# Kernel optimization log

Hardware: AMD Instinct MI355X
Metric: run time of the kernel (lower is better)

Reference implementation:

```python
import jax, jax.numpy as jnp
import numpy as np

DIM, NHEADS, HEAD_DIM = 1536, 12, 128
EPS = 1e-6
ROPE_SPLIT = (22, 21, 21)  # head_dim//2 = 64 -> (c-2*(c//3), c//3, c//3)


def setup_inputs() -> dict:
    key = jax.random.key(0)
    ks = jax.random.split(key, 12)
    B, F, H, W = 1, 8, 16, 28
    L = F * H * W  # 3584
    inp = {
        "x": jax.random.normal(ks[0], (B, L, DIM), jnp.float32),
        "seq_lens": jnp.full((B,), L, dtype=jnp.int64),
        "grid_sizes": jnp.array([[F, H, W]] * B, dtype=jnp.int64),
        "freqs": jax.random.uniform(ks[1], (1024, HEAD_DIM // 2), jnp.float32) * (2 * np.pi),
        "Wq": jax.random.normal(ks[2], (DIM, DIM), jnp.float32) / np.sqrt(DIM),
        "bq": jnp.zeros((DIM,), jnp.float32),
        "Wk": jax.random.normal(ks[3], (DIM, DIM), jnp.float32) / np.sqrt(DIM),
        "bk": jnp.zeros((DIM,), jnp.float32),
        "Wv": jax.random.normal(ks[4], (DIM, DIM), jnp.float32) / np.sqrt(DIM),
        "bv": jnp.zeros((DIM,), jnp.float32),
        "Wo": jax.random.normal(ks[5], (DIM, DIM), jnp.float32) / np.sqrt(DIM),
        "bo": jnp.zeros((DIM,), jnp.float32),
        "gq": jnp.ones((DIM,), jnp.float32),
        "gk": jnp.ones((DIM,), jnp.float32),
    }
    return inp


def _rms_norm(x, g):
    var = jnp.mean(jnp.square(x), axis=-1, keepdims=True)
    return x * jax.lax.rsqrt(var + EPS) * g


def _rope_angles(freqs, F, H, W):
    # freqs: [1024, 64] angles; split per 3D axis and broadcast over the grid
    cf, ch, cw = ROPE_SPLIT
    af = freqs[:F, :cf]
    ah = freqs[:H, cf:cf + ch]
    aw = freqs[:W, cf + ch:]
    ang = jnp.concatenate([
        jnp.broadcast_to(af[:, None, None, :], (F, H, W, cf)),
        jnp.broadcast_to(ah[None, :, None, :], (F, H, W, ch)),
        jnp.broadcast_to(aw[None, None, :, :], (F, H, W, cw)),
    ], axis=-1).reshape(F * H * W, cf + ch + cw)  # [L, 64]
    return jnp.cos(ang), jnp.sin(ang)


def _rope_apply(x, cos, sin):
    # x: [B, L, N, D]; complex multiply by unit-modulus freqs, in real arithmetic
    b, s, n, d = x.shape
    xr = x.reshape(b, s, n, d // 2, 2)
    a, bi = xr[..., 0], xr[..., 1]
    c = cos[None, :, None, :]
    si = sin[None, :, None, :]
    out = jnp.stack([a * c - bi * si, a * si + bi * c], axis=-1)
    return out.reshape(b, s, n, d)


def reference(x, seq_lens, grid_sizes, freqs, Wq, bq, Wk, bk, Wv, bv, Wo, bo, gq, gk):
    b, s, _ = x.shape
    n, d = NHEADS, HEAD_DIM
    gs = np.asarray(grid_sizes)
    F, H, W = int(gs[0, 0]), int(gs[0, 1]), int(gs[0, 2])  # static grid (same per batch)

    q = _rms_norm(x @ Wq + bq, gq).reshape(b, s, n, d)
    k = _rms_norm(x @ Wk + bk, gk).reshape(b, s, n, d)
    v = (x @ Wv + bv).reshape(b, s, n, d)

    cos, sin = _rope_angles(freqs, F, H, W)
    q = _rope_apply(q, cos, sin)
    k = _rope_apply(k, cos, sin)

    # full attention with key-length masking (flash_attention k_lens semantics)
    scale = 1.0 / np.sqrt(d)
    scores = jnp.einsum("bqnd,bknd->bnqk", q, k) * scale
    key_mask = jnp.arange(s)[None, :] < seq_lens[:, None]  # [B, S]
    scores = jnp.where(key_mask[:, None, None, :], scores, -1e9)
    probs = jax.nn.softmax(scores, axis=-1)
    out = jnp.einsum("bnqk,bknd->bqnd", probs, v)

    return out.reshape(b, s, n * d) @ Wo + bo
```

## Files before the change

kernel.cpp:

```cpp
#include <hip/hip_runtime.h>

typedef __bf16 bf16;
typedef __bf16 bf16x8 __attribute__((ext_vector_type(8)));
typedef __bf16 bf16x4 __attribute__((ext_vector_type(4)));
typedef float f32x4 __attribute__((ext_vector_type(4)));

__device__ __forceinline__ void gload_lds16(const void* g, void* l) {
  __builtin_amdgcn_global_load_lds(
      (const __attribute__((address_space(1))) void*)g,
      (__attribute__((address_space(3))) void*)l, 16, 0, 0);
}

__device__ __forceinline__ bf16x8 ld8(const bf16* p) {
  bf16x8 v; __builtin_memcpy(&v, p, 16); return v;
}

__global__ __launch_bounds__(256) void cast_f32_bf16(const float* __restrict__ in,
                                                     bf16* __restrict__ out, int n8) {
  int i = blockIdx.x * 256 + threadIdx.x;
  if (i >= n8) return;
  const float4* p = (const float4*)in + (size_t)i * 2;
  float4 a = p[0], b = p[1];
  bf16x8 o;
  o[0] = (bf16)a.x; o[1] = (bf16)a.y; o[2] = (bf16)a.z; o[3] = (bf16)a.w;
  o[4] = (bf16)b.x; o[5] = (bf16)b.y; o[6] = (bf16)b.z; o[7] = (bf16)b.w;
  *((bf16x8*)out + i) = o;
}

__global__ __launch_bounds__(256) void transpose_w(const float* __restrict__ W,
                                                   bf16* __restrict__ Wt) {
  __shared__ bf16 tile[64][72];
  int t = threadIdx.x;
  int k0 = blockIdx.x * 64, n0 = blockIdx.y * 64;
  int r = t >> 2, c0 = (t & 3) * 16;
  const float* src = W + (size_t)(k0 + r) * 1536 + n0 + c0;
#pragma unroll
  for (int q = 0; q < 4; ++q) {
    float4 v = *(const float4*)(src + q * 4);
    tile[c0 + q * 4 + 0][r] = (bf16)v.x;
    tile[c0 + q * 4 + 1][r] = (bf16)v.y;
    tile[c0 + q * 4 + 2][r] = (bf16)v.z;
    tile[c0 + q * 4 + 3][r] = (bf16)v.w;
  }
  __syncthreads();
  bf16* dst = Wt + (size_t)(n0 + r) * 1536 + k0 + c0;
  bf16x8 o0, o1;
#pragma unroll
  for (int j = 0; j < 8; ++j) { o0[j] = tile[r][c0 + j]; o1[j] = tile[r][c0 + 8 + j]; }
  *(bf16x8*)dst = o0;
  *(bf16x8*)(dst + 8) = o1;
}

__global__ void concat_bias(const float* __restrict__ bq, const float* __restrict__ bk,
                            const float* __restrict__ bv, float* __restrict__ o) {
  int t = blockIdx.x * 256 + threadIdx.x;
  if (t < 1536) o[t] = bq[t];
  else if (t < 3072) o[t] = bk[t - 1536];
  else if (t < 4608) o[t] = bv[t - 3072];
}

template <typename OUT>
__global__ __launch_bounds__(256, 2) void gemm_bt(const bf16* __restrict__ A, const bf16* __restrict__ B,
                                                  const float* __restrict__ bias, OUT* __restrict__ C,
                                                  int M, int N, int K) {
  __shared__ bf16 As[128 * 32], Bs[128 * 32];
  int t = threadIdx.x, l = t & 63, w = t >> 6;
  int lane15 = l & 15, lhi = l >> 4;
  int m0 = blockIdx.x * 128, n0 = blockIdx.y * 128;
  int wm = (w >> 1) * 64, wn = (w & 1) * 64;
  f32x4 zero = {0.f, 0.f, 0.f, 0.f};
  f32x4 acc[4][4];
#pragma unroll
  for (int i = 0; i < 4; ++i)
#pragma unroll
    for (int j = 0; j < 4; ++j) acc[i][j] = zero;

  int srow = t >> 2, scol = (t & 3) * 8;
  const bf16* gA0 = A + (size_t)(m0 + srow) * K + scol;
  const bf16* gA1 = A + (size_t)(m0 + 64 + srow) * K + scol;
  const bf16* gB0 = B + (size_t)(n0 + srow) * K + scol;
  const bf16* gB1 = B + (size_t)(n0 + 64 + srow) * K + scol;
  char* ldsA = (char*)As + (size_t)w * 1024;
  char* ldsB = (char*)Bs + (size_t)w * 1024;

  for (int kt = 0; kt < K; kt += 32) {
    gload_lds16(gA0 + kt, ldsA);
    gload_lds16(gA1 + kt, ldsA + 4096);
    gload_lds16(gB0 + kt, ldsB);
    gload_lds16(gB1 + kt, ldsB + 4096);
    __syncthreads();
    bf16x8 af[4], bfr[4];
#pragma unroll
    for (int i = 0; i < 4; ++i) {
      af[i]  = ld8(&As[(wm + i * 16 + lane15) * 32 + lhi * 8]);
      bfr[i] = ld8(&Bs[(wn + i * 16 + lane15) * 32 + lhi * 8]);
    }
#pragma unroll
    for (int i = 0; i < 4; ++i)
#pragma unroll
      for (int j = 0; j < 4; ++j)
        acc[i][j] = __builtin_amdgcn_mfma_f32_16x16x32_bf16(af[i], bfr[j], acc[i][j], 0, 0, 0);
    __syncthreads();
  }
#pragma unroll
  for (int i = 0; i < 4; ++i)
#pragma unroll
    for (int j = 0; j < 4; ++j) {
      int col = n0 + wn + j * 16 + lane15;
      float bb = bias[col];
#pragma unroll
      for (int r = 0; r < 4; ++r) {
        int row = m0 + wm + i * 16 + lhi * 4 + r;
        C[(size_t)row * N + col] = (OUT)(acc[i][j][r] + bb);
      }
    }
}

__global__ void rope_tab(const float* __restrict__ freqs, const int* __restrict__ gs,
                         float* __restrict__ tabc, float* __restrict__ tabs) {
  int idx = blockIdx.x * 256 + threadIdx.x;
  if (idx >= 3584 * 64) return;
  int s = idx >> 6, i = idx & 63;
  int H = gs[1], W = gs[2];
  int f = s / (H * W);
  int rem = s - f * (H * W);
  int hh = rem / W;
  int ww = rem - hh * W;
  int row = (i < 22) ? f : ((i < 43) ? hh : ww);
  float a = freqs[row * 64 + i];
  tabc[idx] = cosf(a);
  tabs[idx] = sinf(a);
}

__global__ __launch_bounds__(256) void postproc(const bf16* __restrict__ QKV,
    const float* __restrict__ gq, const float* __restrict__ gk,
    const float* __restrict__ tabc, const float* __restrict__ tabs,
    bf16* __restrict__ qb, bf16* __restrict__ kb) {
  int s = blockIdx.x, t = threadIdx.x;
  const bf16* Qr = QKV + (size_t)s * 4608;
  const bf16* Kr = Qr + 1536;
  int j0 = t * 6;
  float qv[6], kv[6];
  float sq = 0.f, sk = 0.f;
#pragma unroll
  for (int j = 0; j < 6; ++j) {
    float a = (float)Qr[j0 + j]; qv[j] = a; sq += a * a;
    float b = (float)Kr[j0 + j]; kv[j] = b; sk += b * b;
  }
#pragma unroll
  for (int off = 32; off > 0; off >>= 1) {
    sq += __shfl_down(sq, off);
    sk += __shfl_down(sk, off);
  }
  __shared__ float red[2][4];
  if ((t & 63) == 0) { red[0][t >> 6] = sq; red[1][t >> 6] = sk; }
  __syncthreads();
  float vq = (red[0][0] + red[0][1]) + (red[0][2] + red[0][3]);
  float vk = (red[1][0] + red[1][1]) + (red[1][2] + red[1][3]);
  float rq = 1.0f / sqrtf(vq * (1.0f / 1536.0f) + 1e-6f);
  float rk = 1.0f / sqrtf(vk * (1.0f / 1536.0f) + 1e-6f);
#pragma unroll
  for (int j = 0; j < 6; j += 2) {
    int jj = j0 + j;
    int d = jj & 127, i = d >> 1, h = jj >> 7;
    float c = tabc[s * 64 + i], sn = tabs[s * 64 + i];
    size_t base = (((size_t)h * 3584 + s) << 7) + d;
    float a = qv[j] * rq * gq[jj], b = qv[j + 1] * rq * gq[jj + 1];
    qb[base] = (bf16)(a * c - b * sn);
    qb[base + 1] = (bf16)(a * sn + b * c);
    float ak = kv[j] * rk * gk[jj], bk2 = kv[j + 1] * rk * gk[jj + 1];
    kb[base] = (bf16)(ak * c - bk2 * sn);
    kb[base + 1] = (bf16)(ak * sn + bk2 * c);
  }
}

__global__ __launch_bounds__(256) void transpose_v(const bf16* __restrict__ QKV,
                                                   bf16* __restrict__ vT) {
  __shared__ bf16 tile[128][72];
  int t = threadIdx.x;
  int h = blockIdx.y;
  int s0 = blockIdx.x * 64;
  int r = t >> 2, c0 = (t & 3) * 32;
  const bf16* src = QKV + (size_t)(s0 + r) * 4608 + 3072 + h * 128 + c0;
#pragma unroll
  for (int q = 0; q < 4; ++q) {
    bf16x8 v = ld8(src + q * 8);
#pragma unroll
    for (int j = 0; j < 8; ++j) tile[c0 + q * 8 + j][r] = v[j];
  }
  __syncthreads();
  int d = t >> 1, sp = (t & 1) * 32;
  bf16* dst = vT + (size_t)(h * 128 + d) * 3584 + s0 + sp;
#pragma unroll
  for (int q = 0; q < 4; ++q) {
    bf16x8 o;
#pragma unroll
    for (int j = 0; j < 8; ++j) o[j] = tile[d][sp + q * 8 + j];
    *(bf16x8*)(dst + q * 8) = o;
  }
}

__global__ __launch_bounds__(256, 2) void flash_attn(
    const bf16* __restrict__ qb, const bf16* __restrict__ kb, const bf16* __restrict__ vT,
    const int* __restrict__ sl, float* __restrict__ po0, float* __restrict__ po1,
    float* __restrict__ po2, float* __restrict__ po3, float* __restrict__ ml) {
  const int L = 3584;
  __shared__ bf16 Ks[2][64 * 128];
  __shared__ bf16 Vs[2][128 * 64];
  int t = threadIdx.x, l = t & 63, w = t >> 6;
  int lane15 = l & 15, lhi = l >> 4;
  int grp48 = l & 48;
  int h = blockIdx.y, z = blockIdx.z;
  int qw = blockIdx.x * 128 + w * 32;
  int seqlen = sl[0];
  const float scale = 0.08838834764831845f;
  float* po = (z == 0) ? po0 : (z == 1) ? po1 : (z == 2) ? po2 : po3;
  float* mlz = ml + (size_t)z * 12 * L * 2;

  bf16x8 aq[2][4];
#pragma unroll
  for (int qf = 0; qf < 2; ++qf)
#pragma unroll
    for (int kc = 0; kc < 4; ++kc)
      aq[qf][kc] = ld8(qb + (((size_t)h * L + qw + qf * 16 + lane15) << 7) + kc * 32 + lhi * 8);

  f32x4 zero = {0.f, 0.f, 0.f, 0.f};
  f32x4 out[2][8];
  float m2[2] = {-1e30f, -1e30f}, ls2[2] = {0.f, 0.f};
#pragma unroll
  for (int qf = 0; qf < 2; ++qf)
#pragma unroll
    for (int df = 0; df < 8; ++df) out[qf][df] = zero;

  int nt = (seqlen + 63) >> 6;
  if (nt > 56) nt = 56;
  int t0 = z * 14, t1 = t0 + 14;
  if (t0 > nt) t0 = nt;
  if (t1 > nt) t1 = nt;

  int rk_s = t >> 4, ck_s = (t & 15) * 16;
  int rv_s = t >> 3;
  int mm = t & 7;
  int sA = 32 * (mm >> 2) + 16 * (mm & 1) + 4 * ((mm >> 1) & 1);
  int oA = 2 * sA;
  int swzk = (rk_s & 7) << 4;
  int swzv = (rv_s & 7) << 4;

  bf16x8 kreg[4], vreg[4];
  if (t0 < t1) {
    int kv0 = t0 * 64;
#pragma unroll
    for (int p = 0; p < 4; ++p) {
      kreg[p] = ld8(kb + (((size_t)h * L + kv0 + p * 16 + rk_s) << 7) + (ck_s >> 1));
      vreg[p] = ld8(vT + (size_t)(h * 128 + p * 32 + rv_s) * L + kv0 + mm * 8);
    }
  }

  int buf = 0;
  for (int ti = t0; ti < t1; ++ti) {
    int kv0 = ti * 64;
#pragma unroll
    for (int p = 0; p < 4; ++p) {
      __builtin_memcpy((char*)Ks[buf] + (p * 16 + rk_s) * 256 + (ck_s ^ swzk), &kreg[p], 16);
      bf16x4 lo, hi;
#pragma unroll
      for (int j = 0; j < 4; ++j) { lo[j] = vreg[p][j]; hi[j] = vreg[p][j + 4]; }
      char* vrow = (char*)Vs[buf] + (p * 32 + rv_s) * 128;
      __builtin_memcpy(vrow + (oA ^ swzv), &lo, 8);
      __builtin_memcpy(vrow + ((oA + 16) ^ swzv), &hi, 8);
    }
    if (ti + 1 < t1) {
      int kn = (ti + 1) * 64;
#pragma unroll
      for (int p = 0; p < 4; ++p) {
        kreg[p] = ld8(kb + (((size_t)h * L + kn + p * 16 + rk_s) << 7) + (ck_s >> 1));
        vreg[p] = ld8(vT + (size_t)(h * 128 + p * 32 + rv_s) * L + kn + mm * 8);
      }
    }
    __syncthreads();

    f32x4 sc[2][4];
#pragma unroll
    for (int qf = 0; qf < 2; ++qf)
#pragma unroll
      for (int a = 0; a < 4; ++a) sc[qf][a] = zero;
#pragma unroll
    for (int a = 0; a < 4; ++a) {
      int rk = a * 16 + lane15;
      const char* krow = (const char*)Ks[buf] + rk * 256;
      int swz = (rk & 7) << 4;
#pragma unroll
      for (int kc = 0; kc < 4; ++kc) {
        bf16x8 bk_ = ld8((const bf16*)(krow + ((kc * 64 + lhi * 16) ^ swz)));
        sc[0][a] = __builtin_amdgcn_mfma_f32_16x16x32_bf16(bk_, aq[0][kc], sc[0][a], 0, 0, 0);
        sc[1][a] = __builtin_amdgcn_mfma_f32_16x16x32_bf16(bk_, aq[1][kc], sc[1][a], 0, 0, 0);
      }
    }

    bool full = (kv0 + 64 <= seqlen);
    bf16x8 ap[2][2];
#pragma unroll
    for (int qf = 0; qf < 2; ++qf) {
      float tm = -1e30f;
#pragma unroll
      for (int a = 0; a < 4; ++a)
#pragma unroll
        for (int r = 0; r < 4; ++r) {
          float s = sc[qf][a][r] * scale;
          if (!full) {
            int col = kv0 + a * 16 + lhi * 4 + r;
            s = (col < seqlen) ? s : -1e30f;
          }
          sc[qf][a][r] = s;
          tm = fmaxf(tm, s);
        }
      tm = fmaxf(tm, __shfl_xor(tm, 16));
      tm = fmaxf(tm, __shfl_xor(tm, 32));
      if (!__all(tm <= m2[qf] + 8.0f)) {
        float nm = fmaxf(m2[qf], tm);
        float f = __expf(m2[qf] - nm);
        m2[qf] = nm;
        ls2[qf] *= f;
#pragma unroll
        for (int r = 0; r < 4; ++r) {
          float fr = __shfl(f, grp48 | (lhi * 4 + r));
#pragma unroll
          for (int df = 0; df < 8; ++df) out[qf][df][r] *= fr;
        }
      }
      float psum = 0.f;
#pragma unroll
      for (int a = 0; a < 4; ++a)
#pragma unroll
        for (int r = 0; r < 4; ++r) {
          float p = __expf(sc[qf][a][r] - m2[qf]);
          sc[qf][a][r] = p;
          psum += p;
        }
      psum += __shfl_xor(psum, 16);
      psum += __shfl_xor(psum, 32);
      ls2[qf] += psum;
#pragma unroll
      for (int c = 0; c < 2; ++c) {
        bf16x8 f8;
#pragma unroll
        for (int r = 0; r < 4; ++r) {
          f8[r] = (bf16)sc[qf][2 * c][r];
          f8[r + 4] = (bf16)sc[qf][2 * c + 1][r];
        }
        ap[qf][c] = f8;
      }
    }

#pragma unroll
    for (int df = 0; df < 8; ++df) {
      int rd = df * 16 + lane15;
      const char* vrow2 = (const char*)Vs[buf] + rd * 128;
      int swz = (rd & 7) << 4;
#pragma unroll
      for (int c = 0; c < 2; ++c) {
        bf16x8 bv_ = ld8((const bf16*)(vrow2 + ((c * 64 + lhi * 16) ^ swz)));
        out[0][df] = __builtin_amdgcn_mfma_f32_16x16x32_bf16(ap[0][c], bv_, out[0][df], 0, 0, 0);
        out[1][df] = __builtin_amdgcn_mfma_f32_16x16x32_bf16(ap[1][c], bv_, out[1][df], 0, 0, 0);
      }
    }
    buf ^= 1;
  }

#pragma unroll
  for (int qf = 0; qf < 2; ++qf) {
#pragma unroll
    for (int r = 0; r < 4; ++r) {
      int row = qw + qf * 16 + lhi * 4 + r;
      size_t rbase = ((size_t)h * L + row) << 7;
#pragma unroll
      for (int df = 0; df < 8; ++df)
        po[rbase + df * 16 + lane15] = out[qf][df][r];
    }
    if (lhi == 0) {
      int row = qw + qf * 16 + lane15;
      mlz[(((size_t)h * L + row) << 1)] = m2[qf];
      mlz[(((size_t)h * L + row) << 1) + 1] = ls2[qf];
    }
  }
}

__global__ __launch_bounds__(256) void combine4(
    const float* __restrict__ po0, const float* __restrict__ po1,
    const float* __restrict__ po2, const float* __restrict__ po3,
    const float* __restrict__ ml, bf16* __restrict__ attn) {
  const int L = 3584;
  int row = blockIdx.x * 8 + (threadIdx.x >> 5);
  int c0 = (threadIdx.x & 31) * 4;
  const size_t mls = (size_t)12 * L * 2;
  float m0 = ml[row * 2],           l0 = ml[row * 2 + 1];
  float m1 = ml[mls + row * 2],     l1 = ml[mls + row * 2 + 1];
  float m2 = ml[2 * mls + row * 2], l2 = ml[2 * mls + row * 2 + 1];
  float m3 = ml[3 * mls + row * 2], l3 = ml[3 * mls + row * 2 + 1];
  float M = fmaxf(fmaxf(m0, m1), fmaxf(m2, m3));
  float w0 = __expf(m0 - M), w1 = __expf(m1 - M);
  float w2 = __expf(m2 - M), w3 = __expf(m3 - M);
  float inv = 1.0f / fmaxf(w0 * l0 + w1 * l1 + w2 * l2 + w3 * l3, 1e-30f);
  float4 a = *(const float4*)(po0 + (size_t)row * 128 + c0);
  float4 b = *(const float4*)(po1 + (size_t)row * 128 + c0);
  float4 c = *(const float4*)(po2 + (size_t)row * 128 + c0);
  float4 d = *(const float4*)(po3 + (size_t)row * 128 + c0);
  int h = row / L, s = row % L;
  bf16x4 o;
  o[0] = (bf16)((w0 * a.x + w1 * b.x + w2 * c.x + w3 * d.x) * inv);
  o[1] = (bf16)((w0 * a.y + w1 * b.y + w2 * c.y + w3 * d.y) * inv);
  o[2] = (bf16)((w0 * a.z + w1 * b.z + w2 * c.z + w3 * d.z) * inv);
  o[3] = (bf16)((w0 * a.w + w1 * b.w + w2 * c.w + w3 * d.w) * inv);
  *(bf16x4*)(attn + (size_t)s * 1536 + h * 128 + c0) = o;
}

extern "C" void kernel_launch(void* const* d_in, const int* in_sizes, int n_in,
                              void* d_out, int out_size, void* d_ws, size_t ws_size,
                              hipStream_t stream) {
  const float* x = (const float*)d_in[0];
  const int* seq_lens = (const int*)d_in[1];
  const int* grid_sizes = (const int*)d_in[2];
  const float* freqs = (const float*)d_in[3];
  const float* Wq = (const float*)d_in[4];
  const float* bq = (const float*)d_in[5];
  const float* Wk = (const float*)d_in[6];
  const float* bk = (const float*)d_in[7];
  const float* Wv = (const float*)d_in[8];
  const float* bv = (const float*)d_in[9];
  const float* Wo = (const float*)d_in[10];
  const float* bo = (const float*)d_in[11];
  const float* gq = (const float*)d_in[12];
  const float* gk = (const float*)d_in[13];

  char* ws = (char*)d_ws;
  bf16* x_bf = (bf16*)(ws + 0);
  bf16* wqkvt = (bf16*)(ws + 11010048);
  bf16* wot = (bf16*)(ws + 25165824);
  float* bqkv = (float*)(ws + 29884416);
  bf16* QKV = (bf16*)(ws + 29902848);
  bf16* qb = (bf16*)(ws + 62932992);
  bf16* kb = (bf16*)(ws + 73943040);
  bf16* vT = (bf16*)(ws + 84953088);
  float* tabc = (float*)(ws + 95963136);
  float* tabs = (float*)(ws + 96880640);
  float* po0 = (float*)(ws + 29902848);
  bf16* attn = (bf16*)(ws + 51922944);
  float* po1 = (float*)(ws + 0);
  float* ml  = (float*)(ws + 95963136);
  float* po2 = (float*)(ws + 97798144);
  float* po3 = (float*)(ws + 119818240);

  cast_f32_bf16<<<2688, 256, 0, stream>>>(x, x_bf, 688128);
  transpose_w<<<dim3(24, 24), 256, 0, stream>>>(Wq, wqkvt);
  transpose_w<<<dim3(24, 24), 256, 0, stream>>>(Wk, wqkvt + 1536 * 1536);
  transpose_w<<<dim3(24, 24), 256, 0, stream>>>(Wv, wqkvt + 2 * 1536 * 1536);
  transpose_w<<<dim3(24, 24), 256, 0, stream>>>(Wo, wot);
  concat_bias<<<18, 256, 0, stream>>>(bq, bk, bv, bqkv);
  rope_tab<<<896, 256, 0, stream>>>(freqs, grid_sizes, tabc, tabs);
  gemm_bt<bf16><<<dim3(28, 36), 256, 0, stream>>>(x_bf, wqkvt, bqkv, QKV, 3584, 4608, 1536);
  postproc<<<3584, 256, 0, stream>>>(QKV, gq, gk, tabc, tabs, qb, kb);
  transpose_v<<<dim3(56, 12), 256, 0, stream>>>(QKV, vT);
  flash_attn<<<dim3(28, 12, 4), 256, 0, stream>>>(qb, kb, vT, seq_lens, po0, po1, po2, po3, ml);
  combine4<<<5376, 256, 0, stream>>>(po0, po1, po2, po3, ml, attn);
  gemm_bt<float><<<dim3(28, 12), 256, 0, stream>>>(attn, wot, bo, (float*)d_out, 3584, 1536, 1536);
}
```

Baseline: 281.5 us.

## Pre-permute V layout, single-buffer LDS, fold softmax scale into Q, bf16 partials

The V transpose kernel now writes V in the permuted column order the attention kernel needs, so the flash kernel can store V into LDS with one 16-byte write instead of two 8-byte scattered writes. The LDS K/V buffers go from double to single buffering with an extra barrier per tile, which halves shared memory and may raise occupancy but adds a sync. The softmax scale is folded into the Q RMS norm factor, removing a multiply per score. Split-K partial outputs are stored as bf16 instead of fp32, halving the partial write and combine read traffic at some precision cost.

```diff
diff --git a/kernel.cpp b/kernel.cpp
--- a/kernel.cpp
+++ b/kernel.cpp
@@ -159,6 +159,7 @@
   float vk = (red[1][0] + red[1][1]) + (red[1][2] + red[1][3]);
   float rq = 1.0f / sqrtf(vq * (1.0f / 1536.0f) + 1e-6f);
   float rk = 1.0f / sqrtf(vk * (1.0f / 1536.0f) + 1e-6f);
+  rq *= 0.08838834764831845f;
 #pragma unroll
   for (int j = 0; j < 6; j += 2) {
     int jj = j0 + j;
@@ -189,32 +190,37 @@
     for (int j = 0; j < 8; ++j) tile[c0 + q * 8 + j][r] = v[j];
   }
   __syncthreads();
-  int d = t >> 1, sp = (t & 1) * 32;
-  bf16* dst = vT + (size_t)(h * 128 + d) * 3584 + s0 + sp;
+  int d = t >> 1, spHalf = t & 1;
+  bf16* dstBase = vT + (size_t)(h * 128 + d) * 3584 + s0;
 #pragma unroll
   for (int q = 0; q < 4; ++q) {
-    bf16x8 o;
-#pragma unroll
-    for (int j = 0; j < 8; ++j) o[j] = tile[d][sp + q * 8 + j];
-    *(bf16x8*)(dst + q * 8) = o;
+    int mm = spHalf * 4 + q;
+    int sA = 32 * (mm >> 2) + 16 * (mm & 1) + 4 * ((mm >> 1) & 1);
+    bf16x4 lo, hi;
+#pragma unroll
+    for (int j = 0; j < 4; ++j) {
+      lo[j] = tile[d][spHalf * 32 + q * 8 + j];
+      hi[j] = tile[d][spHalf * 32 + q * 8 + 4 + j];
+    }
+    *(bf16x4*)(dstBase + sA) = lo;
+    *(bf16x4*)(dstBase + sA + 8) = hi;
   }
 }
 
 __global__ __launch_bounds__(256, 2) void flash_attn(
     const bf16* __restrict__ qb, const bf16* __restrict__ kb, const bf16* __restrict__ vT,
-    const int* __restrict__ sl, float* __restrict__ po0, float* __restrict__ po1,
-    float* __restrict__ po2, float* __restrict__ po3, float* __restrict__ ml) {
+    const int* __restrict__ sl, bf16* __restrict__ po0, bf16* __restrict__ po1,
+    bf16* __restrict__ po2, bf16* __restrict__ po3, float* __restrict__ ml) {
   const int L = 3584;
-  __shared__ bf16 Ks[2][64 * 128];
-  __shared__ bf16 Vs[2][128 * 64];
+  __shared__ bf16 Ks[64 * 128];
+  __shared__ bf16 Vs[128 * 64];
   int t = threadIdx.x, l = t & 63, w = t >> 6;
   int lane15 = l & 15, lhi = l >> 4;
   int grp48 = l & 48;
   int h = blockIdx.y, z = blockIdx.z;
   int qw = blockIdx.x * 128 + w * 32;
   int seqlen = sl[0];
-  const float scale = 0.08838834764831845f;
-  float* po = (z == 0) ? po0 : (z == 1) ? po1 : (z == 2) ? po2 : po3;
+  bf16* po = (z == 0) ? po0 : (z == 1) ? po1 : (z == 2) ? po2 : po3;
   float* mlz = ml + (size_t)z * 12 * L * 2;
 
   bf16x8 aq[2][4];
@@ -239,10 +245,7 @@
   if (t1 > nt) t1 = nt;
 
   int rk_s = t >> 4, ck_s = (t & 15) * 16;
-  int rv_s = t >> 3;
-  int mm = t & 7;
-  int sA = 32 * (mm >> 2) + 16 * (mm & 1) + 4 * ((mm >> 1) & 1);
-  int oA = 2 * sA;
+  int rv_s = t >> 3, cv_s = (t & 7) * 16;
   int swzk = (rk_s & 7) << 4;
   int swzv = (rv_s & 7) << 4;
 
@@ -252,29 +255,23 @@
 #pragma unroll
     for (int p = 0; p < 4; ++p) {
       kreg[p] = ld8(kb + (((size_t)h * L + kv0 + p * 16 + rk_s) << 7) + (ck_s >> 1));
-      vreg[p] = ld8(vT + (size_t)(h * 128 + p * 32 + rv_s) * L + kv0 + mm * 8);
-    }
-  }
-
-  int buf = 0;
+      vreg[p] = ld8(vT + (size_t)(h * 128 + p * 32 + rv_s) * L + kv0 + (cv_s >> 1));
+    }
+  }
+
   for (int ti = t0; ti < t1; ++ti) {
     int kv0 = ti * 64;
 #pragma unroll
     for (int p = 0; p < 4; ++p) {
-      __builtin_memcpy((char*)Ks[buf] + (p * 16 + rk_s) * 256 + (ck_s ^ swzk), &kreg[p], 16);
-      bf16x4 lo, hi;
-#pragma unroll
-      for (int j = 0; j < 4; ++j) { lo[j] = vreg[p][j]; hi[j] = vreg[p][j + 4]; }
-      char* vrow = (char*)Vs[buf] + (p * 32 + rv_s) * 128;
-      __builtin_memcpy(vrow + (oA ^ swzv), &lo, 8);
-      __builtin_memcpy(vrow + ((oA + 16) ^ swzv), &hi, 8);
+      __builtin_memcpy((char*)Ks + (p * 16 + rk_s) * 256 + (ck_s ^ swzk), &kreg[p], 16);
+      __builtin_memcpy((char*)Vs + (p * 32 + rv_s) * 128 + (cv_s ^ swzv), &vreg[p], 16);
     }
     if (ti + 1 < t1) {
       int kn = (ti + 1) * 64;
 #pragma unroll
       for (int p = 0; p < 4; ++p) {
         kreg[p] = ld8(kb + (((size_t)h * L + kn + p * 16 + rk_s) << 7) + (ck_s >> 1));
-        vreg[p] = ld8(vT + (size_t)(h * 128 + p * 32 + rv_s) * L + kn + mm * 8);
+        vreg[p] = ld8(vT + (size_t)(h * 128 + p * 32 + rv_s) * L + kn + (cv_s >> 1));
       }
     }
     __syncthreads();
@@ -287,7 +284,7 @@
 #pragma unroll
     for (int a = 0; a < 4; ++a) {
       int rk = a * 16 + lane15;
-      const char* krow = (const char*)Ks[buf] + rk * 256;
+      const char* krow = (const char*)Ks + rk * 256;
       int swz = (rk & 7) << 4;
 #pragma unroll
       for (int kc = 0; kc < 4; ++kc) {
@@ -306,12 +303,12 @@
       for (int a = 0; a < 4; ++a)
 #pragma unroll
         for (int r = 0; r < 4; ++r) {
-          float s = sc[qf][a][r] * scale;
+          float s = sc[qf][a][r];
           if (!full) {
             int col = kv0 + a * 16 + lhi * 4 + r;
             s = (col < seqlen) ? s : -1e30f;
+            sc[qf][a][r] = s;
           }
-          sc[qf][a][r] = s;
           tm = fmaxf(tm, s);
         }
       tm = fmaxf(tm, __shfl_xor(tm, 16));
@@ -355,7 +352,7 @@
 #pragma unroll
     for (int df = 0; df < 8; ++df) {
       int rd = df * 16 + lane15;
-      const char* vrow2 = (const char*)Vs[buf] + rd * 128;
+      const char* vrow2 = (const char*)Vs + rd * 128;
       int swz = (rd & 7) << 4;
 #pragma unroll
       for (int c = 0; c < 2; ++c) {
@@ -364,7 +361,7 @@
         out[1][df] = __builtin_amdgcn_mfma_f32_16x16x32_bf16(ap[1][c], bv_, out[1][df], 0, 0, 0);
       }
     }
-    buf ^= 1;
+    __syncthreads();
   }
 
 #pragma unroll
@@ -375,7 +372,7 @@
       size_t rbase = ((size_t)h * L + row) << 7;
 #pragma unroll
       for (int df = 0; df < 8; ++df)
-        po[rbase + df * 16 + lane15] = out[qf][df][r];
+        po[rbase + df * 16 + lane15] = (bf16)out[qf][df][r];
     }
     if (lhi == 0) {
       int row = qw + qf * 16 + lane15;
@@ -386,8 +383,8 @@
 }
 
 __global__ __launch_bounds__(256) void combine4(
-    const float* __restrict__ po0, const float* __restrict__ po1,
-    const float* __restrict__ po2, const float* __restrict__ po3,
+    const bf16* __restrict__ po0, const bf16* __restrict__ po1,
+    const bf16* __restrict__ po2, const bf16* __restrict__ po3,
     const float* __restrict__ ml, bf16* __restrict__ attn) {
   const int L = 3584;
   int row = blockIdx.x * 8 + (threadIdx.x >> 5);
@@ -401,16 +398,16 @@
   float w0 = __expf(m0 - M), w1 = __expf(m1 - M);
   float w2 = __expf(m2 - M), w3 = __expf(m3 - M);
   float inv = 1.0f / fmaxf(w0 * l0 + w1 * l1 + w2 * l2 + w3 * l3, 1e-30f);
-  float4 a = *(const float4*)(po0 + (size_t)row * 128 + c0);
-  float4 b = *(const float4*)(po1 + (size_t)row * 128 + c0);
-  float4 c = *(const float4*)(po2 + (size_t)row * 128 + c0);
-  float4 d = *(const float4*)(po3 + (size_t)row * 128 + c0);
+  bf16x4 a, b, c, d;
+  __builtin_memcpy(&a, po0 + (size_t)row * 128 + c0, 8);
+  __builtin_memcpy(&b, po1 + (size_t)row * 128 + c0, 8);
+  __builtin_memcpy(&c, po2 + (size_t)row * 128 + c0, 8);
+  __builtin_memcpy(&d, po3 + (size_t)row * 128 + c0, 8);
   int h = row / L, s = row % L;
   bf16x4 o;
-  o[0] = (bf16)((w0 * a.x + w1 * b.x + w2 * c.x + w3 * d.x) * inv);
-  o[1] = (bf16)((w0 * a.y + w1 * b.y + w2 * c.y + w3 * d.y) * inv);
-  o[2] = (bf16)((w0 * a.z + w1 * b.z + w2 * c.z + w3 * d.z) * inv);
-  o[3] = (bf16)((w0 * a.w + w1 * b.w + w2 * c.w + w3 * d.w) * inv);
+#pragma unroll
+  for (int j = 0; j < 4; ++j)
+    o[j] = (bf16)((w0 * (float)a[j] + w1 * (float)b[j] + w2 * (float)c[j] + w3 * (float)d[j]) * inv);
   *(bf16x4*)(attn + (size_t)s * 1536 + h * 128 + c0) = o;
 }
 
@@ -443,12 +440,12 @@
   bf16* vT = (bf16*)(ws + 84953088);
   float* tabc = (float*)(ws + 95963136);
   float* tabs = (float*)(ws + 96880640);
-  float* po0 = (float*)(ws + 29902848);
+  bf16* po0 = (bf16*)(ws + 29902848);
   bf16* attn = (bf16*)(ws + 51922944);
-  float* po1 = (float*)(ws + 0);
+  bf16* po1 = (bf16*)(ws + 0);
+  bf16* po2 = (bf16*)(ws + 11010048);
   float* ml  = (float*)(ws + 95963136);
-  float* po2 = (float*)(ws + 97798144);
-  float* po3 = (float*)(ws + 119818240);
+  bf16* po3 = (bf16*)(ws + 97798144);
 
   cast_f32_bf16<<<2688, 256, 0, stream>>>(x, x_bf, 688128);
   transpose_w<<<dim3(24, 24), 256, 0, stream>>>(Wq, wqkvt);
```

Result: faster. 275.3 us (-2.2%).
